# Optimization experiments

Measured on AMD Instinct MI355X. Metric: run time of the kernel, lower is better.

Reference implementation:

```python
import jax, jax.numpy as jnp
import numpy as np

WINDOW = 8


def _one_hot_kernel(window):
    # kernel[i//w, i%w, 0, i] = 1 -> extracts each pixel of a w*w sliding window
    k = np.zeros((window, window, 1, window * window), dtype=np.float32)
    for i in range(window * window):
        k[i // window, i % window, 0, i] = 1.0
    return jnp.asarray(k)


def setup_inputs() -> dict:
    key = jax.random.key(0)
    inputs = jax.random.normal(key, (8, 512, 512, 1), dtype=jnp.float32)
    kernel = _one_hot_kernel(WINDOW)  # (8, 8, 1, 64), HWIO
    return {"inputs": inputs, "kernel": kernel}


def reference(inputs, kernel):
    # Faithful translation of keras.backend.conv2d(inputs, kernel):
    # VALID padding, stride 1, NHWC data / HWIO kernel.
    # Mathematically this is im2col/unfold: out[b,h,w,i] = inputs[b, h+i//W, w+i%W, 0].
    y = jax.lax.conv_general_dilated(
        inputs, kernel,
        window_strides=(1, 1),
        padding="VALID",
        dimension_numbers=("NHWC", "HWIO", "NHWC"),
    )
    return y  # (B, H-7, W-7, 64)
```

## Files before the change

kernel.cpp:

```cpp
#include <hip/hip_runtime.h>


#define BATCH   8
#define W_IN    512
#define HW_OUT  505
#define ROW4    (HW_OUT * 16)
#define SEGS    16
#define SEG4    512
#define TILES   (BATCH * HW_OUT * SEGS)
#define SW      40

typedef float f32x4 __attribute__((ext_vector_type(4)));

__global__ __launch_bounds__(256) void unfold_tile_kernel(
    const float* __restrict__ in, float* __restrict__ out)
{
    __shared__ float sm[8 * SW];

    f32x4* __restrict__ out4 = reinterpret_cast<f32x4*>(out);

    for (int tile = blockIdx.x; tile < TILES; tile += gridDim.x) {
        int bh  = tile >> 4;
        int seg = tile & 15;
        int b   = bh / HW_OUT;
        int h   = bh - b * HW_OUT;
        int w0  = seg << 5;

        const float* __restrict__ row_base = in + (b * W_IN + h) * W_IN;

        for (int s = threadIdx.x; s < 8 * SW; s += 256) {
            int r   = s / SW;
            int j   = s - r * SW;
            int col = w0 + j;
            sm[s] = (col < W_IN) ? row_base[(r << 9) + col] : 0.0f;
        }
        __syncthreads();

        int n4 = SEG4;
        if (seg == SEGS - 1) n4 = ROW4 - (SEGS - 1) * SEG4;
        f32x4* __restrict__ o = out4 + (size_t)bh * ROW4 + seg * SEG4;

        for (int t = threadIdx.x; t < n4; t += 256) {
            int i4 = t & 15;
            int p  = t >> 4;
            int r  = i4 >> 1;
            int c  = (i4 & 1) << 2;

            const float* __restrict__ s = &sm[r * SW + p + c];
            f32x4 v;
            v.x = s[0];
            v.y = s[1];
            v.z = s[2];
            v.w = s[3];
            o[t] = v;
        }
        __syncthreads();
    }
}

extern "C" void kernel_launch(void* const* d_in, const int* in_sizes, int n_in,
                              void* d_out, int out_size, void* d_ws, size_t ws_size,
                              hipStream_t stream)
{
    const float* in  = (const float*)d_in[0];
    float*       out = (float*)d_out;

    const int grid = 2048;
    unfold_tile_kernel<<<grid, 256, 0, stream>>>(in, out);
}
```

Baseline: 114.0 us.

## Double-buffer shared-memory staging and widen tiles to 128 output pixels

Splits each output row into 4 segments of 128 pixels instead of 16 of 32, which cuts the redundant halo loads from 40/32 to 136/128. It also adds a two-buffer shared-memory pipeline so the next tile's global loads are issued before the current tile is stored, keeping one barrier per iteration. The kernel is store-bandwidth bound (about 520MB written), so the benefit may be small. Larger tiles also mean fewer tiles per block iteration, which leaves some load imbalance with a grid of 2048.

```diff
diff --git a/kernel.cpp b/kernel.cpp
--- a/kernel.cpp
+++ b/kernel.cpp
@@ -4,57 +4,67 @@
 #define BATCH   8
 #define W_IN    512
 #define HW_OUT  505
-#define ROW4    (HW_OUT * 16)
-#define SEGS    16
-#define SEG4    512
+#define SEGS    4
+#define SEGPIX  128
 #define TILES   (BATCH * HW_OUT * SEGS)
-#define SW      40
+#define SW      136
+#define SMSZ    (8 * SW)
 
 typedef float f32x4 __attribute__((ext_vector_type(4)));
 
-__global__ __launch_bounds__(256) void unfold_tile_kernel(
+__global__ __launch_bounds__(256) void unfold_dbuf_kernel(
     const float* __restrict__ in, float* __restrict__ out)
 {
-    __shared__ float sm[8 * SW];
+    __shared__ float sm[2][SMSZ];
 
     f32x4* __restrict__ out4 = reinterpret_cast<f32x4*>(out);
 
-    for (int tile = blockIdx.x; tile < TILES; tile += gridDim.x) {
-        int bh  = tile >> 4;
-        int seg = tile & 15;
+    auto stage = [&](int t, float* dst) {
+        int bh  = t >> 2;
+        int seg = t & 3;
         int b   = bh / HW_OUT;
         int h   = bh - b * HW_OUT;
-        int w0  = seg << 5;
+        const float* __restrict__ rb = in + (b * W_IN + h) * W_IN + (seg << 7);
+        int maxj = W_IN - (seg << 7);
+        for (int s = threadIdx.x; s < SMSZ; s += 256) {
+            int r = s / SW;
+            int j = s - r * SW;
+            dst[s] = (j < maxj) ? rb[(r << 9) + j] : 0.0f;
+        }
+    };
 
-        const float* __restrict__ row_base = in + (b * W_IN + h) * W_IN;
-
-        for (int s = threadIdx.x; s < 8 * SW; s += 256) {
-            int r   = s / SW;
-            int j   = s - r * SW;
-            int col = w0 + j;
-            sm[s] = (col < W_IN) ? row_base[(r << 9) + col] : 0.0f;
-        }
-        __syncthreads();
-
-        int n4 = SEG4;
-        if (seg == SEGS - 1) n4 = ROW4 - (SEGS - 1) * SEG4;
-        f32x4* __restrict__ o = out4 + (size_t)bh * ROW4 + seg * SEG4;
-
-        for (int t = threadIdx.x; t < n4; t += 256) {
-            int i4 = t & 15;
-            int p  = t >> 4;
+    auto store_tile = [&](int t, const float* smb) {
+        int bh  = t >> 2;
+        int seg = t & 3;
+        int n4  = ((seg == 3) ? (HW_OUT - 3 * SEGPIX) : SEGPIX) << 4;
+        f32x4* __restrict__ o = out4 + (size_t)bh * (HW_OUT * 16) + (seg << 11);
+        for (int q = threadIdx.x; q < n4; q += 256) {
+            int i4 = q & 15;
+            int p  = q >> 4;
             int r  = i4 >> 1;
             int c  = (i4 & 1) << 2;
-
-            const float* __restrict__ s = &sm[r * SW + p + c];
+            const float* __restrict__ s = smb + r * SW + p + c;
             f32x4 v;
             v.x = s[0];
             v.y = s[1];
             v.z = s[2];
             v.w = s[3];
-            o[t] = v;
+            o[q] = v;
         }
+    };
+
+    int tile = blockIdx.x;
+    if (tile >= TILES) return;
+    stage(tile, sm[0]);
+    int cur = 0;
+    for (;;) {
+        int next = tile + gridDim.x;
         __syncthreads();
+        if (next < TILES) stage(next, sm[cur ^ 1]);
+        store_tile(tile, sm[cur]);
+        if (next >= TILES) break;
+        tile = next;
+        cur ^= 1;
     }
 }
 
@@ -66,5 +76,5 @@
     float*       out = (float*)d_out;
 
     const int grid = 2048;
-    unfold_tile_kernel<<<grid, 256, 0, stream>>>(in, out);
+    unfold_dbuf_kernel<<<grid, 256, 0, stream>>>(in, out);
 }
```

Result: faster. 105.5 us (-7.5%).
